# Kernel tuning notes

Hardware: AMD Instinct MI355X
Metric: run time of the kernel (lower is better)

Reference implementation:

```python
import jax, jax.numpy as jnp
import numpy as np

H = 16  # num_heads


def setup_inputs() -> dict:
    key = jax.random.key(0)
    ks = jax.random.split(key, 12)
    B, L, E = 2, 2048, 1024
    s = 1.0 / np.sqrt(E)
    inp = {
        "query": jax.random.normal(ks[0], (B, L, E), jnp.float32),
        "key": jax.random.normal(ks[1], (B, L, E), jnp.float32),
        "value": jax.random.normal(ks[2], (B, L, E), jnp.float32),
        "Wq": jax.random.normal(ks[3], (E, E), jnp.float32) * s,
        "bq": jnp.zeros((E,), jnp.float32),
        "Wk": jax.random.normal(ks[4], (E, E), jnp.float32) * s,
        "bk": jnp.zeros((E,), jnp.float32),
        "Wv": jax.random.normal(ks[5], (E, E), jnp.float32) * s,
        "bv": jnp.zeros((E,), jnp.float32),
        "Wo": jax.random.normal(ks[6], (E, E), jnp.float32) * s,
        "bo": jnp.zeros((E,), jnp.float32),
    }
    return inp


def _split_heads(x, h):
    B, L, E = x.shape
    return x.reshape(B, L, h, E // h).transpose(0, 2, 1, 3)  # [B,h,L,d]


def reference(query, key, value, Wq, bq, Wk, bk, Wv, bv, Wo, bo):
    B, L, E = query.shape
    d = E // H
    q = _split_heads(query @ Wq.T + bq, H)
    k = _split_heads(key @ Wk.T + bk, H)
    v = _split_heads(value @ Wv.T + bv, H)
    scores = jnp.einsum("bhqd,bhkd->bhqk", q, k) / jnp.sqrt(jnp.float32(d))
    weights = jax.nn.softmax(scores, axis=-1)  # [B,h,L,L]
    # dropout is identity in eval mode (deterministic reference)
    Z = jnp.einsum("bhqk,bhkd->bhqd", weights, v)
    Z = Z.transpose(0, 2, 1, 3).reshape(B, L, E)
    out = Z @ Wo.T + bo
    return out, weights
```

## Files before the change

kernel.cpp:

```cpp
#include <hip/hip_runtime.h>

typedef _Float16 half8 __attribute__((ext_vector_type(8)));
typedef _Float16 half4 __attribute__((ext_vector_type(4)));
typedef float floatx4 __attribute__((ext_vector_type(4)));

__device__ __forceinline__ int lds_off(int row, int chunk) {
    return row * 32 + ((chunk ^ (row & 3)) << 3);
}

__device__ __forceinline__ void ld16f(float* d, const float* s) {
    *(float4*)(d + 0)  = *(const float4*)(s + 0);
    *(float4*)(d + 4)  = *(const float4*)(s + 4);
    *(float4*)(d + 8)  = *(const float4*)(s + 8);
    *(float4*)(d + 12) = *(const float4*)(s + 12);
}

__device__ __forceinline__ void cvt16(half8& h0, half8& h1, const float* f) {
#pragma unroll
    for (int i = 0; i < 8; i++) { h0[i] = (_Float16)f[i]; h1[i] = (_Float16)f[8 + i]; }
}

__global__ __launch_bounds__(256) void gemm_qkv(
    const float* __restrict__ q, const float* __restrict__ k, const float* __restrict__ v,
    const float* __restrict__ Wq, const float* __restrict__ Wk, const float* __restrict__ Wv,
    const float* __restrict__ bq, const float* __restrict__ bk, const float* __restrict__ bv,
    _Float16* __restrict__ outQ, _Float16* __restrict__ outK, _Float16* __restrict__ outVt)
{
    __shared__ __align__(16) _Float16 sA[128 * 32];
    __shared__ __align__(16) _Float16 sB[128 * 32];

    const int t = threadIdx.x;
    const int tileN = blockIdx.x * 128;
    const int tileM = blockIdx.y * 128;
    const int z = blockIdx.z;

    const float* Ab = (z == 0) ? q : (z == 1 ? k : v);
    const float* Bb = (z == 0) ? Wq : (z == 1 ? Wk : Wv);
    const float* bias = (z == 0) ? bq : (z == 1 ? bk : bv);

    const int srow = t >> 1, shalf = t & 1, c0 = shalf * 2;
    const int lane = t & 63, wave = t >> 6;
    const int wm = (wave >> 1) * 64, wn = (wave & 1) * 64;
    const int l15 = lane & 15, quad = lane >> 4;

    const float* Arow = Ab + (long)(tileM + srow) * 1024 + shalf * 16;
    const float* Brow = Bb + (long)(tileN + srow) * 1024 + shalf * 16;

    float fA[16], fB[16];
    ld16f(fA, Arow);
    ld16f(fB, Brow);

    floatx4 acc[4][4];
#pragma unroll
    for (int i = 0; i < 4; i++)
#pragma unroll
        for (int j = 0; j < 4; j++)
            acc[i][j] = (floatx4){0.f, 0.f, 0.f, 0.f};

    for (int it = 0; it < 32; ++it) {
        __syncthreads();
        {
            half8 h0, h1;
            cvt16(h0, h1, fA);
            *(half8*)&sA[lds_off(srow, c0)]     = h0;
            *(half8*)&sA[lds_off(srow, c0 + 1)] = h1;
            cvt16(h0, h1, fB);
            *(half8*)&sB[lds_off(srow, c0)]     = h0;
            *(half8*)&sB[lds_off(srow, c0 + 1)] = h1;
        }
        __syncthreads();
        if (it + 1 < 32) {
            const int k1 = (it + 1) << 5;
            ld16f(fA, Arow + k1);
            ld16f(fB, Brow + k1);
        }
        half8 af[4], bf[4];
#pragma unroll
        for (int i = 0; i < 4; i++) af[i] = *(const half8*)&sA[lds_off(wm + i * 16 + l15, quad)];
#pragma unroll
        for (int j = 0; j < 4; j++) bf[j] = *(const half8*)&sB[lds_off(wn + j * 16 + l15, quad)];
#pragma unroll
        for (int i = 0; i < 4; i++)
#pragma unroll
            for (int j = 0; j < 4; j++)
                acc[i][j] = __builtin_amdgcn_mfma_f32_16x16x32_f16(af[i], bf[j], acc[i][j], 0, 0, 0);
    }

#pragma unroll
    for (int i = 0; i < 4; i++) {
#pragma unroll
        for (int j = 0; j < 4; j++) {
            const int row0 = tileM + wm + i * 16 + quad * 4;
            const int col  = tileN + wn + j * 16 + l15;
            if (z == 2) {
                half4 hv;
#pragma unroll
                for (int r = 0; r < 4; r++) hv[r] = (_Float16)(acc[i][j][r] + bias[col]);
                const int bh = ((row0 >> 11) << 4) + (col >> 6);
                *(half4*)&outVt[(long)bh * 131072 + (long)(col & 63) * 2048 + (row0 & 2047)] = hv;
            } else {
                _Float16* dst = z ? outK : outQ;
#pragma unroll
                for (int r = 0; r < 4; r++) {
                    const int row = row0 + r;
                    dst[(long)(((row >> 11) << 4) + (col >> 6)) * 131072 + (long)(row & 2047) * 64 + (col & 63)] =
                        (_Float16)(acc[i][j][r] + bias[col]);
                }
            }
        }
    }
}

__global__ __launch_bounds__(256) void gemm_out(
    const _Float16* __restrict__ A, const float* __restrict__ B,
    const float* __restrict__ bias, float* __restrict__ C)
{
    __shared__ __align__(16) _Float16 sA[128 * 32];
    __shared__ __align__(16) _Float16 sB[128 * 32];

    const int t = threadIdx.x;
    const int tileN = blockIdx.x * 128;
    const int tileM = blockIdx.y * 128;

    const int srow = t >> 1, shalf = t & 1, c0 = shalf * 2;
    const int lane = t & 63, wave = t >> 6;
    const int wm = (wave >> 1) * 64, wn = (wave & 1) * 64;
    const int l15 = lane & 15, quad = lane >> 4;

    const _Float16* Arow = A + (long)(tileM + srow) * 1024 + shalf * 16;
    const float*    Brow = B + (long)(tileN + srow) * 1024 + shalf * 16;

    half8 hA[2];
    float fB[16];
    hA[0] = *(const half8*)Arow;
    hA[1] = *(const half8*)(Arow + 8);
    ld16f(fB, Brow);

    floatx4 acc[4][4];
#pragma unroll
    for (int i = 0; i < 4; i++)
#pragma unroll
        for (int j = 0; j < 4; j++)
            acc[i][j] = (floatx4){0.f, 0.f, 0.f, 0.f};

    for (int it = 0; it < 32; ++it) {
        __syncthreads();
        {
            *(half8*)&sA[lds_off(srow, c0)]     = hA[0];
            *(half8*)&sA[lds_off(srow, c0 + 1)] = hA[1];
            half8 h0, h1;
            cvt16(h0, h1, fB);
            *(half8*)&sB[lds_off(srow, c0)]     = h0;
            *(half8*)&sB[lds_off(srow, c0 + 1)] = h1;
        }
        __syncthreads();
        if (it + 1 < 32) {
            const int k1 = (it + 1) << 5;
            hA[0] = *(const half8*)(Arow + k1);
            hA[1] = *(const half8*)(Arow + k1 + 8);
            ld16f(fB, Brow + k1);
        }
        half8 af[4], bf[4];
#pragma unroll
        for (int i = 0; i < 4; i++) af[i] = *(const half8*)&sA[lds_off(wm + i * 16 + l15, quad)];
#pragma unroll
        for (int j = 0; j < 4; j++) bf[j] = *(const half8*)&sB[lds_off(wn + j * 16 + l15, quad)];
#pragma unroll
        for (int i = 0; i < 4; i++)
#pragma unroll
            for (int j = 0; j < 4; j++)
                acc[i][j] = __builtin_amdgcn_mfma_f32_16x16x32_f16(af[i], bf[j], acc[i][j], 0, 0, 0);
    }

#pragma unroll
    for (int i = 0; i < 4; i++)
#pragma unroll
        for (int j = 0; j < 4; j++)
#pragma unroll
            for (int r = 0; r < 4; r++) {
                const int row = tileM + wm + i * 16 + quad * 4 + r;
                const int col = tileN + wn + j * 16 + l15;
                C[(long)row * 1024 + col] = acc[i][j][r] + bias[col];
            }
}

__global__ __launch_bounds__(256, 2) void attn_fused(
    const _Float16* __restrict__ Q,
    const _Float16* __restrict__ K,
    const _Float16* __restrict__ Vt,
    float* __restrict__ W,
    _Float16* __restrict__ Z)
{
    __shared__ __align__(16) _Float16 sK[128 * 64];
    __shared__ __align__(16) _Float16 sV[64 * 128];
    __shared__ __align__(16) _Float16 sP[128 * 128];

    const int t = threadIdx.x;
    const int tileM = blockIdx.x * 128;
    const int bh = blockIdx.y;
    const int lane = t & 63, wave = t >> 6;
    const int l15 = lane & 15, quad = lane >> 4;
    const int wm = wave * 32;

    const _Float16* Qb = Q + (long)bh * 131072;
    const _Float16* Kb = K + (long)bh * 131072;
    const _Float16* Vb = Vt + (long)bh * 131072;
    float* Wb = W + (long)bh * 4194304;

    const int krow = t >> 1, khalf = t & 1;
    const int vrow = t >> 2, vq = t & 3;

    half8 qf[2][2];
#pragma unroll
    for (int i = 0; i < 2; i++)
#pragma unroll
        for (int kk = 0; kk < 2; kk++)
            qf[i][kk] = *(const half8*)(Qb + (long)(tileM + wm + i * 16 + l15) * 64 + kk * 32 + quad * 8);

    float m[2][4], l[2][4];
#pragma unroll
    for (int i = 0; i < 2; i++)
#pragma unroll
        for (int r = 0; r < 4; r++) { m[i][r] = -__builtin_inff(); l[i][r] = 0.f; }

    const _Float16* Ksrc = Kb + (long)krow * 64 + khalf * 32;
    const _Float16* Vsrc = Vb + (long)vrow * 2048;

    half8 kr[4], vr[4];
#pragma unroll
    for (int c = 0; c < 4; c++) kr[c] = *(const half8*)(Ksrc + c * 8);

    for (int kv = 0; kv < 2048; kv += 128) {
        __syncthreads();
#pragma unroll
        for (int c = 0; c < 4; c++)
            *(half8*)&sK[krow * 64 + (((khalf * 4 + c) ^ (krow & 7)) << 3)] = kr[c];
        __syncthreads();
        if (kv + 128 < 2048) {
#pragma unroll
            for (int c = 0; c < 4; c++) kr[c] = *(const half8*)(Ksrc + (long)(kv + 128) * 64 + c * 8);
        }

        floatx4 acc[2][8];
#pragma unroll
        for (int i = 0; i < 2; i++)
#pragma unroll
            for (int j = 0; j < 8; j++) acc[i][j] = (floatx4){0.f, 0.f, 0.f, 0.f};

#pragma unroll
        for (int kk = 0; kk < 2; kk++) {
#pragma unroll
            for (int j = 0; j < 8; j++) {
                const int row = j * 16 + l15;
                half8 bf = *(const half8*)&sK[row * 64 + (((kk * 4 + quad) ^ (row & 7)) << 3)];
                acc[0][j] = __builtin_amdgcn_mfma_f32_16x16x32_f16(qf[0][kk], bf, acc[0][j], 0, 0, 0);
                acc[1][j] = __builtin_amdgcn_mfma_f32_16x16x32_f16(qf[1][kk], bf, acc[1][j], 0, 0, 0);
            }
        }

#pragma unroll
        for (int i = 0; i < 2; i++)
#pragma unroll
            for (int r = 0; r < 4; r++) {
                float tmax = acc[i][0][r];
#pragma unroll
                for (int j = 1; j < 8; j++) tmax = fmaxf(tmax, acc[i][j][r]);
#pragma unroll
                for (int off = 1; off < 16; off <<= 1) tmax = fmaxf(tmax, __shfl_xor(tmax, off));
                const float mn = fmaxf(m[i][r], tmax * 0.125f);
                const float corr = __expf(m[i][r] - mn);
                float ts = 0.f;
#pragma unroll
                for (int j = 0; j < 8; j++) ts += __expf(acc[i][j][r] * 0.125f - mn);
#pragma unroll
                for (int off = 1; off < 16; off <<= 1) ts += __shfl_xor(ts, off);
                l[i][r] = l[i][r] * corr + ts;
                m[i][r] = mn;
            }
    }

#pragma unroll
    for (int i = 0; i < 2; i++)
#pragma unroll
        for (int r = 0; r < 4; r++) l[i][r] = 1.f / l[i][r];

    floatx4 accz[2][4];
#pragma unroll
    for (int i = 0; i < 2; i++)
#pragma unroll
        for (int j = 0; j < 4; j++) accz[i][j] = (floatx4){0.f, 0.f, 0.f, 0.f};

#pragma unroll
    for (int c = 0; c < 4; c++) kr[c] = *(const half8*)(Ksrc + c * 8);
#pragma unroll
    for (int c = 0; c < 4; c++) vr[c] = *(const half8*)(Vsrc + (vq + c * 4) * 8);

    for (int kv = 0; kv < 2048; kv += 128) {
        __syncthreads();
#pragma unroll
        for (int c = 0; c < 4; c++)
            *(half8*)&sK[krow * 64 + (((khalf * 4 + c) ^ (krow & 7)) << 3)] = kr[c];
#pragma unroll
        for (int c = 0; c < 4; c++) {
            const int ch = vq + c * 4;
            *(half8*)&sV[vrow * 128 + ((ch ^ (vrow & 15)) << 3)] = vr[c];
        }
        __syncthreads();
        if (kv + 128 < 2048) {
#pragma unroll
            for (int c = 0; c < 4; c++) kr[c] = *(const half8*)(Ksrc + (long)(kv + 128) * 64 + c * 8);
#pragma unroll
            for (int c = 0; c < 4; c++) vr[c] = *(const half8*)(Vsrc + kv + 128 + (vq + c * 4) * 8);
        }

        floatx4 acc[2][8];
#pragma unroll
        for (int i = 0; i < 2; i++)
#pragma unroll
            for (int j = 0; j < 8; j++) acc[i][j] = (floatx4){0.f, 0.f, 0.f, 0.f};

#pragma unroll
        for (int kk = 0; kk < 2; kk++) {
#pragma unroll
            for (int j = 0; j < 8; j++) {
                const int row = j * 16 + l15;
                half8 bf = *(const half8*)&sK[row * 64 + (((kk * 4 + quad) ^ (row & 7)) << 3)];
                acc[0][j] = __builtin_amdgcn_mfma_f32_16x16x32_f16(qf[0][kk], bf, acc[0][j], 0, 0, 0);
                acc[1][j] = __builtin_amdgcn_mfma_f32_16x16x32_f16(qf[1][kk], bf, acc[1][j], 0, 0, 0);
            }
        }

#pragma unroll
        for (int i = 0; i < 2; i++) {
#pragma unroll
            for (int r = 0; r < 4; r++) {
                const int q = wm + i * 16 + quad * 4 + r;
                float* wr = Wb + (long)(tileM + q) * 2048 + kv + l15;
                _Float16* sprow = &sP[q * 128 + (l15 & 7)];
                const int qx = q & 15;
                const int hi = l15 >> 3;
#pragma unroll
                for (int j = 0; j < 8; j++) {
                    const float p = __expf(acc[i][j][r] * 0.125f - m[i][r]) * l[i][r];
                    __builtin_nontemporal_store(p, wr + j * 16);
                    sprow[((j * 2 + hi) ^ qx) << 3] = (_Float16)p;
                }
            }
        }
        __syncthreads();

#pragma unroll
        for (int kk = 0; kk < 4; kk++) {
            half8 pf[2];
#pragma unroll
            for (int i = 0; i < 2; i++) {
                const int q = wm + i * 16 + l15;
                pf[i] = *(const half8*)&sP[q * 128 + (((kk * 4 + quad) ^ (q & 15)) << 3)];
            }
#pragma unroll
            for (int j = 0; j < 4; j++) {
                const int d = j * 16 + l15;
                half8 vf = *(const half8*)&sV[d * 128 + (((kk * 4 + quad) ^ (d & 15)) << 3)];
                accz[0][j] = __builtin_amdgcn_mfma_f32_16x16x32_f16(pf[0], vf, accz[0][j], 0, 0, 0);
                accz[1][j] = __builtin_amdgcn_mfma_f32_16x16x32_f16(pf[1], vf, accz[1][j], 0, 0, 0);
            }
        }
    }

    const int bb = bh >> 4, hd = bh & 15;
#pragma unroll
    for (int i = 0; i < 2; i++)
#pragma unroll
        for (int j = 0; j < 4; j++)
#pragma unroll
            for (int r = 0; r < 4; r++)
                Z[(long)(bb * 2048 + tileM + wm + i * 16 + quad * 4 + r) * 1024 + hd * 64 + j * 16 + l15] =
                    (_Float16)accz[i][j][r];
}

extern "C" void kernel_launch(void* const* d_in, const int* in_sizes, int n_in,
                              void* d_out, int out_size, void* d_ws, size_t ws_size,
                              hipStream_t stream) {
    (void)in_sizes; (void)n_in; (void)out_size; (void)ws_size;
    const float* query = (const float*)d_in[0];
    const float* key   = (const float*)d_in[1];
    const float* value = (const float*)d_in[2];
    const float* Wq = (const float*)d_in[3];
    const float* bq = (const float*)d_in[4];
    const float* Wk = (const float*)d_in[5];
    const float* bk = (const float*)d_in[6];
    const float* Wv = (const float*)d_in[7];
    const float* bv = (const float*)d_in[8];
    const float* Wo = (const float*)d_in[9];
    const float* bo = (const float*)d_in[10];

    _Float16* wsQ  = (_Float16*)d_ws;
    _Float16* wsK  = wsQ + 4194304;
    _Float16* wsVt = wsK + 4194304;
    _Float16* wsZ  = wsVt + 4194304;

    float* outF = (float*)d_out;
    float* Wgt  = outF + 4194304;

    dim3 blk(256);
    gemm_qkv<<<dim3(8, 32, 3), blk, 0, stream>>>(query, key, value, Wq, Wk, Wv, bq, bk, bv, wsQ, wsK, wsVt);
    attn_fused<<<dim3(16, 32), blk, 0, stream>>>(wsQ, wsK, wsVt, Wgt, wsZ);
    gemm_out<<<dim3(8, 32), blk, 0, stream>>>(wsZ, Wo, bo, outF);
}
```

Baseline: 850.8 us.

## Double-buffer GEMM LDS, alias attention P buffer to cut LDS, swap grid order

Both GEMM kernels now use double-buffered LDS tiles with a two-step register prefetch, so each iteration needs one barrier instead of two. The attention kernel drops its dedicated P buffer and reuses the K/V region plus a smaller extra area as per-wave P scratch. This lowers LDS use so launch bounds can raise occupancy to 3 blocks per CU, and the V prefetch moves later in the loop. The grid axes are swapped in all three launches, which changes block scheduling order and L2 reuse. The risks are higher register pressure at 3 waves and an extra barrier in the attention loop.

```diff
diff --git a/kernel.cpp b/kernel.cpp
--- a/kernel.cpp
+++ b/kernel.cpp
@@ -26,12 +26,12 @@
     const float* __restrict__ bq, const float* __restrict__ bk, const float* __restrict__ bv,
     _Float16* __restrict__ outQ, _Float16* __restrict__ outK, _Float16* __restrict__ outVt)
 {
-    __shared__ __align__(16) _Float16 sA[128 * 32];
-    __shared__ __align__(16) _Float16 sB[128 * 32];
+    __shared__ __align__(16) _Float16 sA[2][128 * 32];
+    __shared__ __align__(16) _Float16 sB[2][128 * 32];
 
     const int t = threadIdx.x;
-    const int tileN = blockIdx.x * 128;
-    const int tileM = blockIdx.y * 128;
+    const int tileM = blockIdx.x * 128;
+    const int tileN = blockIdx.y * 128;
     const int z = blockIdx.z;
 
     const float* Ab = (z == 0) ? q : (z == 1 ? k : v);
@@ -49,6 +49,18 @@
     float fA[16], fB[16];
     ld16f(fA, Arow);
     ld16f(fB, Brow);
+    {
+        half8 h0, h1;
+        cvt16(h0, h1, fA);
+        *(half8*)&sA[0][lds_off(srow, c0)]     = h0;
+        *(half8*)&sA[0][lds_off(srow, c0 + 1)] = h1;
+        cvt16(h0, h1, fB);
+        *(half8*)&sB[0][lds_off(srow, c0)]     = h0;
+        *(half8*)&sB[0][lds_off(srow, c0 + 1)] = h1;
+    }
+    ld16f(fA, Arow + 32);
+    ld16f(fB, Brow + 32);
+    __syncthreads();
 
     floatx4 acc[4][4];
 #pragma unroll
@@ -58,32 +70,31 @@
             acc[i][j] = (floatx4){0.f, 0.f, 0.f, 0.f};
 
     for (int it = 0; it < 32; ++it) {
-        __syncthreads();
-        {
+        const int cur = it & 1;
+        half8 af[4], bf[4];
+#pragma unroll
+        for (int i = 0; i < 4; i++) af[i] = *(const half8*)&sA[cur][lds_off(wm + i * 16 + l15, quad)];
+#pragma unroll
+        for (int j = 0; j < 4; j++) bf[j] = *(const half8*)&sB[cur][lds_off(wn + j * 16 + l15, quad)];
+        if (it + 1 < 32) {
             half8 h0, h1;
             cvt16(h0, h1, fA);
-            *(half8*)&sA[lds_off(srow, c0)]     = h0;
-            *(half8*)&sA[lds_off(srow, c0 + 1)] = h1;
+            *(half8*)&sA[cur ^ 1][lds_off(srow, c0)]     = h0;
+            *(half8*)&sA[cur ^ 1][lds_off(srow, c0 + 1)] = h1;
             cvt16(h0, h1, fB);
-            *(half8*)&sB[lds_off(srow, c0)]     = h0;
-            *(half8*)&sB[lds_off(srow, c0 + 1)] = h1;
-        }
-        __syncthreads();
-        if (it + 1 < 32) {
-            const int k1 = (it + 1) << 5;
-            ld16f(fA, Arow + k1);
-            ld16f(fB, Brow + k1);
-        }
-        half8 af[4], bf[4];
-#pragma unroll
-        for (int i = 0; i < 4; i++) af[i] = *(const half8*)&sA[lds_off(wm + i * 16 + l15, quad)];
-#pragma unroll
-        for (int j = 0; j < 4; j++) bf[j] = *(const half8*)&sB[lds_off(wn + j * 16 + l15, quad)];
+            *(half8*)&sB[cur ^ 1][lds_off(srow, c0)]     = h0;
+            *(half8*)&sB[cur ^ 1][lds_off(srow, c0 + 1)] = h1;
+        }
+        if (it + 2 < 32) {
+            ld16f(fA, Arow + (it + 2) * 32);
+            ld16f(fB, Brow + (it + 2) * 32);
+        }
 #pragma unroll
         for (int i = 0; i < 4; i++)
 #pragma unroll
             for (int j = 0; j < 4; j++)
                 acc[i][j] = __builtin_amdgcn_mfma_f32_16x16x32_f16(af[i], bf[j], acc[i][j], 0, 0, 0);
+        __syncthreads();
     }
 
 #pragma unroll
@@ -115,12 +126,12 @@
     const _Float16* __restrict__ A, const float* __restrict__ B,
     const float* __restrict__ bias, float* __restrict__ C)
 {
-    __shared__ __align__(16) _Float16 sA[128 * 32];
-    __shared__ __align__(16) _Float16 sB[128 * 32];
+    __shared__ __align__(16) _Float16 sA[2][128 * 32];
+    __shared__ __align__(16) _Float16 sB[2][128 * 32];
 
     const int t = threadIdx.x;
-    const int tileN = blockIdx.x * 128;
-    const int tileM = blockIdx.y * 128;
+    const int tileM = blockIdx.x * 128;
+    const int tileN = blockIdx.y * 128;
 
     const int srow = t >> 1, shalf = t & 1, c0 = shalf * 2;
     const int lane = t & 63, wave = t >> 6;
@@ -135,6 +146,18 @@
     hA[0] = *(const half8*)Arow;
     hA[1] = *(const half8*)(Arow + 8);
     ld16f(fB, Brow);
+    {
+        *(half8*)&sA[0][lds_off(srow, c0)]     = hA[0];
+        *(half8*)&sA[0][lds_off(srow, c0 + 1)] = hA[1];
+        half8 h0, h1;
+        cvt16(h0, h1, fB);
+        *(half8*)&sB[0][lds_off(srow, c0)]     = h0;
+        *(half8*)&sB[0][lds_off(srow, c0 + 1)] = h1;
+    }
+    hA[0] = *(const half8*)(Arow + 32);
+    hA[1] = *(const half8*)(Arow + 40);
+    ld16f(fB, Brow + 32);
+    __syncthreads();
 
     floatx4 acc[4][4];
 #pragma unroll
@@ -144,32 +167,32 @@
             acc[i][j] = (floatx4){0.f, 0.f, 0.f, 0.f};
 
     for (int it = 0; it < 32; ++it) {
-        __syncthreads();
-        {
-            *(half8*)&sA[lds_off(srow, c0)]     = hA[0];
-            *(half8*)&sA[lds_off(srow, c0 + 1)] = hA[1];
+        const int cur = it & 1;
+        half8 af[4], bf[4];
+#pragma unroll
+        for (int i = 0; i < 4; i++) af[i] = *(const half8*)&sA[cur][lds_off(wm + i * 16 + l15, quad)];
+#pragma unroll
+        for (int j = 0; j < 4; j++) bf[j] = *(const half8*)&sB[cur][lds_off(wn + j * 16 + l15, quad)];
+        if (it + 1 < 32) {
+            *(half8*)&sA[cur ^ 1][lds_off(srow, c0)]     = hA[0];
+            *(half8*)&sA[cur ^ 1][lds_off(srow, c0 + 1)] = hA[1];
             half8 h0, h1;
             cvt16(h0, h1, fB);
-            *(half8*)&sB[lds_off(srow, c0)]     = h0;
-            *(half8*)&sB[lds_off(srow, c0 + 1)] = h1;
-        }
-        __syncthreads();
-        if (it + 1 < 32) {
-            const int k1 = (it + 1) << 5;
-            hA[0] = *(const half8*)(Arow + k1);
-            hA[1] = *(const half8*)(Arow + k1 + 8);
-            ld16f(fB, Brow + k1);
-        }
-        half8 af[4], bf[4];
-#pragma unroll
-        for (int i = 0; i < 4; i++) af[i] = *(const half8*)&sA[lds_off(wm + i * 16 + l15, quad)];
-#pragma unroll
-        for (int j = 0; j < 4; j++) bf[j] = *(const half8*)&sB[lds_off(wn + j * 16 + l15, quad)];
+            *(half8*)&sB[cur ^ 1][lds_off(srow, c0)]     = h0;
+            *(half8*)&sB[cur ^ 1][lds_off(srow, c0 + 1)] = h1;
+        }
+        if (it + 2 < 32) {
+            const int k2 = (it + 2) << 5;
+            hA[0] = *(const half8*)(Arow + k2);
+            hA[1] = *(const half8*)(Arow + k2 + 8);
+            ld16f(fB, Brow + k2);
+        }
 #pragma unroll
         for (int i = 0; i < 4; i++)
 #pragma unroll
             for (int j = 0; j < 4; j++)
                 acc[i][j] = __builtin_amdgcn_mfma_f32_16x16x32_f16(af[i], bf[j], acc[i][j], 0, 0, 0);
+        __syncthreads();
     }
 
 #pragma unroll
@@ -184,23 +207,24 @@
             }
 }
 
-__global__ __launch_bounds__(256, 2) void attn_fused(
+__global__ __launch_bounds__(256, 3) void attn_fused(
     const _Float16* __restrict__ Q,
     const _Float16* __restrict__ K,
     const _Float16* __restrict__ Vt,
     float* __restrict__ W,
     _Float16* __restrict__ Z)
 {
-    __shared__ __align__(16) _Float16 sK[128 * 64];
-    __shared__ __align__(16) _Float16 sV[64 * 128];
-    __shared__ __align__(16) _Float16 sP[128 * 128];
+    __shared__ __align__(16) _Float16 S[24576];
+    _Float16* sK = S;
+    _Float16* sV = S + 8192;
 
     const int t = threadIdx.x;
-    const int tileM = blockIdx.x * 128;
-    const int bh = blockIdx.y;
+    const int bh = blockIdx.x;
+    const int tileM = blockIdx.y * 128;
     const int lane = t & 63, wave = t >> 6;
     const int l15 = lane & 15, quad = lane >> 4;
     const int wm = wave * 32;
+    _Float16* myP = (wave < 2) ? (S + wave * 4096) : (S + 16384 + (wave - 2) * 4096);
 
     const _Float16* Qb = Q + (long)bh * 131072;
     const _Float16* Kb = K + (long)bh * 131072;
@@ -226,7 +250,7 @@
     const _Float16* Ksrc = Kb + (long)krow * 64 + khalf * 32;
     const _Float16* Vsrc = Vb + (long)vrow * 2048;
 
-    half8 kr[4], vr[4];
+    half8 kr[4];
 #pragma unroll
     for (int c = 0; c < 4; c++) kr[c] = *(const half8*)(Ksrc + c * 8);
 
@@ -292,6 +316,7 @@
 
 #pragma unroll
     for (int c = 0; c < 4; c++) kr[c] = *(const half8*)(Ksrc + c * 8);
+    half8 vr[4];
 #pragma unroll
     for (int c = 0; c < 4; c++) vr[c] = *(const half8*)(Vsrc + (vq + c * 4) * 8);
 
@@ -309,8 +334,6 @@
         if (kv + 128 < 2048) {
 #pragma unroll
             for (int c = 0; c < 4; c++) kr[c] = *(const half8*)(Ksrc + (long)(kv + 128) * 64 + c * 8);
-#pragma unroll
-            for (int c = 0; c < 4; c++) vr[c] = *(const half8*)(Vsrc + kv + 128 + (vq + c * 4) * 8);
         }
 
         floatx4 acc[2][8];
@@ -329,15 +352,16 @@
                 acc[1][j] = __builtin_amdgcn_mfma_f32_16x16x32_f16(qf[1][kk], bf, acc[1][j], 0, 0, 0);
             }
         }
+        __syncthreads();
 
 #pragma unroll
         for (int i = 0; i < 2; i++) {
 #pragma unroll
             for (int r = 0; r < 4; r++) {
-                const int q = wm + i * 16 + quad * 4 + r;
-                float* wr = Wb + (long)(tileM + q) * 2048 + kv + l15;
-                _Float16* sprow = &sP[q * 128 + (l15 & 7)];
-                const int qx = q & 15;
+                const int ql = i * 16 + quad * 4 + r;
+                float* wr = Wb + (long)(tileM + wm + ql) * 2048 + kv + l15;
+                _Float16* sprow = myP + ql * 128 + (l15 & 7);
+                const int qx = ql & 15;
                 const int hi = l15 >> 3;
 #pragma unroll
                 for (int j = 0; j < 8; j++) {
@@ -347,15 +371,14 @@
                 }
             }
         }
-        __syncthreads();
 
 #pragma unroll
         for (int kk = 0; kk < 4; kk++) {
             half8 pf[2];
 #pragma unroll
             for (int i = 0; i < 2; i++) {
-                const int q = wm + i * 16 + l15;
-                pf[i] = *(const half8*)&sP[q * 128 + (((kk * 4 + quad) ^ (q & 15)) << 3)];
+                const int ql = i * 16 + l15;
+                pf[i] = *(const half8*)&myP[ql * 128 + (((kk * 4 + quad) ^ (ql & 15)) << 3)];
             }
 #pragma unroll
             for (int j = 0; j < 4; j++) {
@@ -364,6 +387,11 @@
                 accz[0][j] = __builtin_amdgcn_mfma_f32_16x16x32_f16(pf[0], vf, accz[0][j], 0, 0, 0);
                 accz[1][j] = __builtin_amdgcn_mfma_f32_16x16x32_f16(pf[1], vf, accz[1][j], 0, 0, 0);
             }
+        }
+
+        if (kv + 128 < 2048) {
+#pragma unroll
+            for (int c = 0; c < 4; c++) vr[c] = *(const half8*)(Vsrc + kv + 128 + (vq + c * 4) * 8);
         }
     }
 
@@ -403,7 +431,7 @@
     float* Wgt  = outF + 4194304;
 
     dim3 blk(256);
-    gemm_qkv<<<dim3(8, 32, 3), blk, 0, stream>>>(query, key, value, Wq, Wk, Wv, bq, bk, bv, wsQ, wsK, wsVt);
-    attn_fused<<<dim3(16, 32), blk, 0, stream>>>(wsQ, wsK, wsVt, Wgt, wsZ);
-    gemm_out<<<dim3(8, 32), blk, 0, stream>>>(wsZ, Wo, bo, outF);
-}
+    gemm_qkv<<<dim3(32, 8, 3), blk, 0, stream>>>(query, key, value, Wq, Wk, Wv, bq, bk, bv, wsQ, wsK, wsVt);
+    attn_fused<<<dim3(32, 16), blk, 0, stream>>>(wsQ, wsK, wsVt, Wgt, wsZ);
+    gemm_out<<<dim3(32, 8), blk, 0, stream>>>(wsZ, Wo, bo, outF);
+}
```

Measured after the change: 876.3 us. 3.0% more time.
